# Performance work log

Hardware: AMD Instinct MI355X
Metric: run time of the kernel (lower is better)

## Reference

```python
import jax, jax.numpy as jnp
import numpy as np

B, S, D_IN, D_H = 2048, 256, 128, 256
C2 = 2.7193  # time-decay log offset from the original module


def setup_inputs() -> dict:
    key = jax.random.key(0)
    k0, k1, k2, k3 = jax.random.split(key, 4)
    inputs = jax.random.normal(k0, (B, S, D_IN), dtype=jnp.float32)
    # time must be increasing so intervals are positive (log(dt + 2.7193) valid)
    dt = jax.random.uniform(k1, (B, S), minval=0.1, maxval=5.0, dtype=jnp.float32)
    time = jnp.cumsum(dt, axis=1)
    Wi = jax.random.normal(k2, (D_IN, D_H), dtype=jnp.float32) / np.sqrt(D_IN).astype(np.float32)
    bi = jnp.zeros((D_H,), dtype=jnp.float32)
    Wh = jax.random.normal(k3, (D_H, D_H), dtype=jnp.float32) / np.sqrt(D_H).astype(np.float32)
    bh = jnp.zeros((D_H,), dtype=jnp.float32)
    return {"inputs": inputs, "time": time, "Wi": Wi, "bi": bi, "Wh": Wh, "bh": bh}


def reference(inputs, time, Wi, bi, Wh, bh):
    Bsz, Slen, _ = inputs.shape
    H = Wh.shape[0]
    # time points -> intervals, then decay weight 1/log(dt + c2)
    dt = time[:, 1:] - time[:, :-1]                     # [B, S-1]
    w = 1.0 / jnp.log(dt + C2)                          # [B, S-1]
    # precompute all input projections once (original recomputes per gate)
    x_proj = jnp.einsum('bsd,dh->bsh', inputs[:, :-1], Wi) + bi  # [B, S-1, H]

    def step(carry, xs):
        h, c, o = carry
        xz, wt = xs                                     # xz:[B,H], wt:[B]
        z = xz + h @ Wh + bh                            # shared gate pre-activation
        g = jax.nn.sigmoid(z)                           # f_t == i_t == o_t (same linears in source)
        C_bar = jnp.tanh(z)
        C_S = jnp.tanh(c @ Wh + bh)                     # short-term memory
        C_star = (c - C_S) + C_S * wt[:, None]          # long-term + discounted short-term
        c_new = g * C_star + g * C_bar
        h_new = g * jnp.tanh(C_bar)
        return (h_new, c_new, g), None

    zeros = jnp.zeros((Bsz, H), dtype=inputs.dtype)
    (h, c, o), _ = jax.lax.scan(
        step, (zeros, zeros, zeros),
        (jnp.swapaxes(x_proj, 0, 1), w.T),
    )
    res = o @ Wh + bh                                   # linear_hidden(o_t) of last step
    return jnp.stack((res, h, c))                       # [3, B, H]
```

## Files before the change

### kernel.cpp

```cpp
#include <hip/hip_runtime.h>

typedef __attribute__((ext_vector_type(8))) short short8;
typedef __attribute__((ext_vector_type(4))) float floatx4;
typedef __attribute__((ext_vector_type(2))) float floatx2;

#define LOG2E 1.44269504088896340736f

#define BAR() asm volatile("s_waitcnt lgkmcnt(0)\n\ts_barrier" ::: "memory")

__device__ __forceinline__ unsigned short f2bf(float f) {
  unsigned u = __float_as_uint(f);
  u += 0x7FFFu + ((u >> 16) & 1u);
  return (unsigned short)(u >> 16);
}

__device__ __forceinline__ unsigned cvtpk(float lo, float hi) {
  unsigned r;
  asm("v_cvt_pk_bf16_f32 %0, %1, %2" : "=v"(r) : "v"(lo), "v"(hi));
  return r;
}

__device__ __forceinline__ int sidx(int row, int k) {
  return row * 256 + (k ^ ((row & 7) << 3));
}

__global__ __launch_bounds__(1024, 4) void tlstm_kernel(
    const float* __restrict__ x, const float* __restrict__ tim,
    const float* __restrict__ Wi, const float* __restrict__ bi,
    const float* __restrict__ Wh, const float* __restrict__ bh,
    float* __restrict__ out)
{
  __shared__ __align__(16) unsigned short Sst[2 * 4096];
  __shared__ __align__(16) unsigned short Sx[2 * 2048];
  __shared__ float WMt[2048];

  const int tid = threadIdx.x;
  const int wv  = tid >> 6;
  const int l   = tid & 63;
  const int q   = l >> 4;
  const int r   = l & 15;
  const int b0  = blockIdx.x * 8;
  const int col = wv * 16 + r;

  short8 wh[8];
#pragma unroll
  for (int c = 0; c < 8; ++c)
#pragma unroll
    for (int j = 0; j < 8; ++j)
      wh[c][j] = (short)f2bf(Wh[(c * 32 + q * 8 + j) * 256 + col]);
  short8 wi[4];
#pragma unroll
  for (int c = 0; c < 4; ++c)
#pragma unroll
    for (int j = 0; j < 8; ++j)
      wi[c][j] = (short)f2bf(Wi[(c * 32 + q * 8 + j) * 256 + col]);
  const float bhc = bh[col], bic = bi[col];

  const int rbx = (r >> 2) & 1;
  const int Bs  = r * 256 + 8 * (q ^ (r & 3));
  const int raE = Bs + 32 * rbx;
  const int raO = Bs + 32 * (1 - rbx);
  const int Bx  = r * 128 + 8 * (q ^ (r & 3));
  const int xaE = Bx + 32 * rbx;
  const int xaO = Bx + 32 * (1 - rbx);
  const int wr0 = sidx(4 * q,     col), wr1 = sidx(4 * q + 1, col);
  const int wr2 = sidx(4 * q + 2, col), wr3 = sidx(4 * q + 3, col);
  const int xwi = wv * 128 + ((2 * l) ^ ((wv & 7) << 3));
  const float* xp = x + (long)(b0 + (wv >> 1)) * 32768 + (wv & 1) * 128 + l * 2;

  *(unsigned long long*)&Sst[tid * 4] = 0ULL;
  for (int i = tid; i < 2040; i += 1024) {
    int t = i >> 3, bl = i & 7;
    float t0 = tim[(b0 + bl) * 256 + t];
    float t1 = tim[(b0 + bl) * 256 + t + 1];
    WMt[i] = 1.f - 1.f / logf(t1 - t0 + 2.7193f);
  }
  {
    floatx2 v = *(const floatx2*)xp;
    *(unsigned*)&Sx[xwi] = cvtpk(v.x, v.y);
  }
  xp += 256;
  __syncthreads();

  float c0 = 0.f, c1 = 0.f, h0 = 0.f, h1 = 0.f, g0 = 0.f, g1 = 0.f;
  int xro = 0;
  int wmi = 2 * q;

  auto proc1 = [&](float z0, float cp0, float cin, float wmv,
                   float& cno, float& gno, float& hno, int ih, int ic, int woff) {
    float z  = fminf(fmaxf(z0,  -10.f), 10.f);
    float cp = fminf(fmaxf(cp0, -10.f), 10.f);
    float u  = __builtin_amdgcn_exp2f(-LOG2E * z);
    float u2 = u * u;
    float v  = __builtin_amdgcn_exp2f(-2.f * LOG2E * cp);
    float a1 = 1.f + u, a2 = 1.f + u2, a3 = 1.f + v;
    float p12 = a1 * a2;
    float D   = __builtin_amdgcn_rcpf(p12 * a3);
    float Da3 = D * a3;
    float g   = Da3 * a2;
    float ir2 = Da3 * a1;
    float ir3 = D * p12;
    float Cb  = fmaf(-u2, ir2, ir2);
    float Cs  = fmaf(-v, ir3, ir3);
    float Cstar = fmaf(-Cs, wmv, cin);
    float cn = g * (Cstar + Cb);
    float s = Cb * Cb;
    float P = fmaf(0.003592028f, s, -0.008863236f);
    P = fmaf(P, s, 0.021869488f);
    P = fmaf(P, s, -0.053968254f);
    P = fmaf(P, s, 0.133333333f);
    P = fmaf(P, s, -0.333333333f);
    P = fmaf(P, s, 1.0f);
    float hn = g * (Cb * P);
    Sst[woff + ih] = (unsigned short)((__float_as_uint(hn) + 0x8000u) >> 16);
    Sst[woff + ic] = (unsigned short)((__float_as_uint(cn) + 0x8000u) >> 16);
    cno = cn; gno = g; hno = hn;
  };

  auto dostep = [&](int roff, int woff, float xz0, float xz1, int wmoff) {
    short8 sf[8];
    sf[0] = *(const short8*)&Sst[roff + raE];
    sf[1] = *(const short8*)&Sst[roff + raO];
    sf[2] = *(const short8*)&Sst[roff + raE + 64];
    sf[3] = *(const short8*)&Sst[roff + raO + 64];
    sf[4] = *(const short8*)&Sst[roff + raE + 128];
    sf[5] = *(const short8*)&Sst[roff + raO + 128];
    sf[6] = *(const short8*)&Sst[roff + raE + 192];
    sf[7] = *(const short8*)&Sst[roff + raO + 192];
    floatx4 aP = {bhc, bhc, bhc, bhc};
    floatx4 aQ = {0.f, 0.f, 0.f, 0.f};
    aP = __builtin_amdgcn_mfma_f32_16x16x32_bf16(sf[0], wh[0], aP, 0, 0, 0);
    aQ = __builtin_amdgcn_mfma_f32_16x16x32_bf16(sf[1], wh[1], aQ, 0, 0, 0);
    aP = __builtin_amdgcn_mfma_f32_16x16x32_bf16(sf[2], wh[2], aP, 0, 0, 0);
    aQ = __builtin_amdgcn_mfma_f32_16x16x32_bf16(sf[3], wh[3], aQ, 0, 0, 0);
    aP = __builtin_amdgcn_mfma_f32_16x16x32_bf16(sf[4], wh[4], aP, 0, 0, 0);
    aQ = __builtin_amdgcn_mfma_f32_16x16x32_bf16(sf[5], wh[5], aQ, 0, 0, 0);
    aP = __builtin_amdgcn_mfma_f32_16x16x32_bf16(sf[6], wh[6], aP, 0, 0, 0);
    aQ = __builtin_amdgcn_mfma_f32_16x16x32_bf16(sf[7], wh[7], aQ, 0, 0, 0);
    floatx2 wmv = *(const floatx2*)&WMt[wmoff];
    float z0  = aP[0] + aQ[0] + xz0;
    float cp0 = aP[1] + aQ[1];
    float z1  = aP[2] + aQ[2] + xz1;
    float cp1 = aP[3] + aQ[3];
    proc1(z0, cp0, c0, wmv.x, c0, g0, h0, wr0, wr1, woff);
    proc1(z1, cp1, c1, wmv.y, c1, g1, h1, wr2, wr3, woff);
    BAR();
  };

  floatx4 xacc;
  auto loadx = [&]() {
    short8 xf[4];
    xf[0] = *(const short8*)&Sx[xro + xaE];
    xf[1] = *(const short8*)&Sx[xro + xaO];
    xf[2] = *(const short8*)&Sx[xro + xaE + 64];
    xf[3] = *(const short8*)&Sx[xro + xaO + 64];
    floatx4 a = {bic, bic, bic, bic};
    a = __builtin_amdgcn_mfma_f32_16x16x32_bf16(xf[0], wi[0], a, 0, 0, 0);
    a = __builtin_amdgcn_mfma_f32_16x16x32_bf16(xf[1], wi[1], a, 0, 0, 0);
    a = __builtin_amdgcn_mfma_f32_16x16x32_bf16(xf[2], wi[2], a, 0, 0, 0);
    a = __builtin_amdgcn_mfma_f32_16x16x32_bf16(xf[3], wi[3], a, 0, 0, 0);
    xacc = a;
  };

  for (int p = 0; p < 127; ++p) {
    floatx2 nv = *(const floatx2*)xp;
    xp += 256;
    loadx();
    dostep(0, 4096, xacc[0], xacc[2], wmi);
    *(unsigned*)&Sx[(xro ^ 2048) + xwi] = cvtpk(nv.x, nv.y);
    dostep(4096, 0, xacc[1], xacc[3], wmi + 8);
    xro ^= 2048;
    wmi += 16;
  }

  loadx();
  dostep(0, 4096, xacc[0], xacc[2], wmi);

  Sst[wr0] = f2bf(g0);  Sst[wr1] = 0;
  Sst[wr2] = f2bf(g1);  Sst[wr3] = 0;
  BAR();
  short8 gf[8];
  gf[0] = *(const short8*)&Sst[raE];
  gf[1] = *(const short8*)&Sst[raO];
  gf[2] = *(const short8*)&Sst[raE + 64];
  gf[3] = *(const short8*)&Sst[raO + 64];
  gf[4] = *(const short8*)&Sst[raE + 128];
  gf[5] = *(const short8*)&Sst[raO + 128];
  gf[6] = *(const short8*)&Sst[raE + 192];
  gf[7] = *(const short8*)&Sst[raO + 192];
  floatx4 res = {bhc, bhc, bhc, bhc};
#pragma unroll
  for (int c = 0; c < 8; ++c)
    res = __builtin_amdgcn_mfma_f32_16x16x32_bf16(gf[c], wh[c], res, 0, 0, 0);

  const long P  = 2048L * 256;
  const long o0 = (long)(b0 + 2 * q) * 256;
  const long o1 = (long)(b0 + 2 * q + 1) * 256;
  out[o0 + col]         = res[0];
  out[o1 + col]         = res[2];
  out[P + o0 + col]     = h0;
  out[P + o1 + col]     = h1;
  out[2 * P + o0 + col] = c0;
  out[2 * P + o1 + col] = c1;
}

extern "C" void kernel_launch(void* const* d_in, const int* in_sizes, int n_in,
                              void* d_out, int out_size, void* d_ws, size_t ws_size,
                              hipStream_t stream) {
  const float* xin = (const float*)d_in[0];
  const float* tim = (const float*)d_in[1];
  const float* Wi  = (const float*)d_in[2];
  const float* bi  = (const float*)d_in[3];
  const float* Wh  = (const float*)d_in[4];
  const float* bh  = (const float*)d_in[5];
  tlstm_kernel<<<dim3(256), dim3(1024), 0, stream>>>(xin, tim, Wi, bi, Wh, bh, (float*)d_out);
}
```

Before: 272.6 us.

## Halve batch rows per block and give each wave two column tiles

Each block now handles 4 batch rows with 512 threads (8 waves) instead of 8 rows with 1024 threads, and the grid doubles to 512 blocks. Each wave holds two 16-column tiles of Wh and Wi in registers and issues two independent MFMA chains per step, using only half the lanes' results. The aim is cheaper per-step barriers with fewer waves and more blocks spread across CUs. In exchange, half of the MFMA output is wasted and register pressure from the doubled weight fragments rises, which may limit occupancy.

```diff
diff --git a/kernel.cpp b/kernel.cpp
--- a/kernel.cpp
+++ b/kernel.cpp
@@ -20,57 +20,66 @@
   return r;
 }
 
-__device__ __forceinline__ int sidx(int row, int k) {
-  return row * 256 + (k ^ ((row & 7) << 3));
-}
-
-__global__ __launch_bounds__(1024, 4) void tlstm_kernel(
+__global__ __launch_bounds__(512, 4) void tlstm_kernel(
     const float* __restrict__ x, const float* __restrict__ tim,
     const float* __restrict__ Wi, const float* __restrict__ bi,
     const float* __restrict__ Wh, const float* __restrict__ bh,
     float* __restrict__ out)
 {
-  __shared__ __align__(16) unsigned short Sst[2 * 4096];
-  __shared__ __align__(16) unsigned short Sx[2 * 2048];
-  __shared__ float WMt[2048];
+  __shared__ __align__(16) unsigned short Sst[2 * 2048];
+  __shared__ __align__(16) unsigned short Sx[2 * 1024];
+  __shared__ __align__(16) float WMt[1024];
 
   const int tid = threadIdx.x;
   const int wv  = tid >> 6;
   const int l   = tid & 63;
   const int q   = l >> 4;
   const int r   = l & 15;
-  const int b0  = blockIdx.x * 8;
-  const int col = wv * 16 + r;
-
-  short8 wh[8];
-#pragma unroll
-  for (int c = 0; c < 8; ++c)
-#pragma unroll
-    for (int j = 0; j < 8; ++j)
-      wh[c][j] = (short)f2bf(Wh[(c * 32 + q * 8 + j) * 256 + col]);
-  short8 wi[4];
-#pragma unroll
-  for (int c = 0; c < 4; ++c)
-#pragma unroll
-    for (int j = 0; j < 8; ++j)
-      wi[c][j] = (short)f2bf(Wi[(c * 32 + q * 8 + j) * 256 + col]);
-  const float bhc = bh[col], bic = bi[col];
-
-  const int rbx = (r >> 2) & 1;
-  const int Bs  = r * 256 + 8 * (q ^ (r & 3));
-  const int raE = Bs + 32 * rbx;
-  const int raO = Bs + 32 * (1 - rbx);
-  const int Bx  = r * 128 + 8 * (q ^ (r & 3));
-  const int xaE = Bx + 32 * rbx;
-  const int xaO = Bx + 32 * (1 - rbx);
-  const int wr0 = sidx(4 * q,     col), wr1 = sidx(4 * q + 1, col);
-  const int wr2 = sidx(4 * q + 2, col), wr3 = sidx(4 * q + 3, col);
-  const int xwi = wv * 128 + ((2 * l) ^ ((wv & 7) << 3));
+  const int r8  = r & 7;
+  const int qt  = q >> 1;
+  const int q1  = q & 1;
+  const int b0  = blockIdx.x * 4;
+
+  const int col1 = wv * 32 + r;
+  const int col2 = col1 + 16;
+  const int wcol = wv * 32 + qt * 16 + r;
+
+  short8 wh[2][8];
+#pragma unroll
+  for (int tx = 0; tx < 2; ++tx)
+#pragma unroll
+    for (int c = 0; c < 8; ++c)
+#pragma unroll
+      for (int j = 0; j < 8; ++j)
+        wh[tx][c][j] = (short)f2bf(Wh[(c * 32 + q * 8 + j) * 256 + wv * 32 + tx * 16 + r]);
+  short8 wi[2][4];
+#pragma unroll
+  for (int tx = 0; tx < 2; ++tx)
+#pragma unroll
+    for (int c = 0; c < 4; ++c)
+#pragma unroll
+      for (int j = 0; j < 8; ++j)
+        wi[tx][c][j] = (short)f2bf(Wi[(c * 32 + q * 8 + j) * 256 + wv * 32 + tx * 16 + r]);
+  const float bh1 = bh[col1], bh2 = bh[col2];
+  const float bi1 = bi[col1], bi2 = bi[col2];
+
+  const int rbx = r8 >> 2;
+  const int Bs  = r8 * 256 + ((q * 8) ^ ((r8 & 3) << 3));
+  const int raE = Bs + 32 * rbx, raO = Bs + 32 * (1 - rbx);
+  const int Bx  = r8 * 128 + ((q * 8) ^ ((r8 & 3) << 3));
+  const int xaE = Bx + 32 * rbx, xaO = Bx + 32 * (1 - rbx);
+  const int R0 = 4 * q1;
+  const int wr0 = R0 * 256       + (wcol ^ (R0 << 3));
+  const int wr1 = (R0 + 1) * 256 + (wcol ^ ((R0 + 1) << 3));
+  const int wr2 = (R0 + 2) * 256 + (wcol ^ ((R0 + 2) << 3));
+  const int wr3 = (R0 + 3) * 256 + (wcol ^ ((R0 + 3) << 3));
+  const int xwi = wv * 128 + ((2 * l) ^ (wv << 3));
   const float* xp = x + (long)(b0 + (wv >> 1)) * 32768 + (wv & 1) * 128 + l * 2;
+  const int wm2 = 2 * q1;
 
   *(unsigned long long*)&Sst[tid * 4] = 0ULL;
-  for (int i = tid; i < 2040; i += 1024) {
-    int t = i >> 3, bl = i & 7;
+  for (int i = tid; i < 1020; i += 512) {
+    int t = i >> 2, bl = i & 3;
     float t0 = tim[(b0 + bl) * 256 + t];
     float t1 = tim[(b0 + bl) * 256 + t + 1];
     WMt[i] = 1.f - 1.f / logf(t1 - t0 + 2.7193f);
@@ -82,9 +91,9 @@
   xp += 256;
   __syncthreads();
 
-  float c0 = 0.f, c1 = 0.f, h0 = 0.f, h1 = 0.f, g0 = 0.f, g1 = 0.f;
+  float c0s = 0.f, c1s = 0.f, h0 = 0.f, h1 = 0.f, g0 = 0.f, g1 = 0.f;
   int xro = 0;
-  int wmi = 2 * q;
+  int wmi = 0;
 
   auto proc1 = [&](float z0, float cp0, float cin, float wmv,
                    float& cno, float& gno, float& hno, int ih, int ic, int woff) {
@@ -127,81 +136,88 @@
     sf[5] = *(const short8*)&Sst[roff + raO + 128];
     sf[6] = *(const short8*)&Sst[roff + raE + 192];
     sf[7] = *(const short8*)&Sst[roff + raO + 192];
-    floatx4 aP = {bhc, bhc, bhc, bhc};
-    floatx4 aQ = {0.f, 0.f, 0.f, 0.f};
-    aP = __builtin_amdgcn_mfma_f32_16x16x32_bf16(sf[0], wh[0], aP, 0, 0, 0);
-    aQ = __builtin_amdgcn_mfma_f32_16x16x32_bf16(sf[1], wh[1], aQ, 0, 0, 0);
-    aP = __builtin_amdgcn_mfma_f32_16x16x32_bf16(sf[2], wh[2], aP, 0, 0, 0);
-    aQ = __builtin_amdgcn_mfma_f32_16x16x32_bf16(sf[3], wh[3], aQ, 0, 0, 0);
-    aP = __builtin_amdgcn_mfma_f32_16x16x32_bf16(sf[4], wh[4], aP, 0, 0, 0);
-    aQ = __builtin_amdgcn_mfma_f32_16x16x32_bf16(sf[5], wh[5], aQ, 0, 0, 0);
-    aP = __builtin_amdgcn_mfma_f32_16x16x32_bf16(sf[6], wh[6], aP, 0, 0, 0);
-    aQ = __builtin_amdgcn_mfma_f32_16x16x32_bf16(sf[7], wh[7], aQ, 0, 0, 0);
-    floatx2 wmv = *(const floatx2*)&WMt[wmoff];
-    float z0  = aP[0] + aQ[0] + xz0;
-    float cp0 = aP[1] + aQ[1];
-    float z1  = aP[2] + aQ[2] + xz1;
-    float cp1 = aP[3] + aQ[3];
-    proc1(z0, cp0, c0, wmv.x, c0, g0, h0, wr0, wr1, woff);
-    proc1(z1, cp1, c1, wmv.y, c1, g1, h1, wr2, wr3, woff);
+    floatx4 a1 = {bh1, bh1, bh1, bh1};
+    floatx4 a2 = {bh2, bh2, bh2, bh2};
+#pragma unroll
+    for (int c = 0; c < 8; ++c) {
+      a1 = __builtin_amdgcn_mfma_f32_16x16x32_bf16(sf[c], wh[0][c], a1, 0, 0, 0);
+      a2 = __builtin_amdgcn_mfma_f32_16x16x32_bf16(sf[c], wh[1][c], a2, 0, 0, 0);
+    }
+    floatx2 wmv = *(const floatx2*)&WMt[wmoff + wm2];
+    float z0  = (qt ? a2[0] : a1[0]) + xz0;
+    float cp0 =  qt ? a2[1] : a1[1];
+    float z1  = (qt ? a2[2] : a1[2]) + xz1;
+    float cp1 =  qt ? a2[3] : a1[3];
+    proc1(z0, cp0, c0s, wmv.x, c0s, g0, h0, wr0, wr1, woff);
+    proc1(z1, cp1, c1s, wmv.y, c1s, g1, h1, wr2, wr3, woff);
     BAR();
   };
 
-  floatx4 xacc;
+  float xz[4];
   auto loadx = [&]() {
     short8 xf[4];
     xf[0] = *(const short8*)&Sx[xro + xaE];
     xf[1] = *(const short8*)&Sx[xro + xaO];
     xf[2] = *(const short8*)&Sx[xro + xaE + 64];
     xf[3] = *(const short8*)&Sx[xro + xaO + 64];
-    floatx4 a = {bic, bic, bic, bic};
-    a = __builtin_amdgcn_mfma_f32_16x16x32_bf16(xf[0], wi[0], a, 0, 0, 0);
-    a = __builtin_amdgcn_mfma_f32_16x16x32_bf16(xf[1], wi[1], a, 0, 0, 0);
-    a = __builtin_amdgcn_mfma_f32_16x16x32_bf16(xf[2], wi[2], a, 0, 0, 0);
-    a = __builtin_amdgcn_mfma_f32_16x16x32_bf16(xf[3], wi[3], a, 0, 0, 0);
-    xacc = a;
+    floatx4 x1 = {bi1, bi1, bi1, bi1};
+    floatx4 x2 = {bi2, bi2, bi2, bi2};
+#pragma unroll
+    for (int c = 0; c < 4; ++c) {
+      x1 = __builtin_amdgcn_mfma_f32_16x16x32_bf16(xf[c], wi[0][c], x1, 0, 0, 0);
+      x2 = __builtin_amdgcn_mfma_f32_16x16x32_bf16(xf[c], wi[1][c], x2, 0, 0, 0);
+    }
+    xz[0] = qt ? x2[0] : x1[0];
+    xz[1] = qt ? x2[1] : x1[1];
+    xz[2] = qt ? x2[2] : x1[2];
+    xz[3] = qt ? x2[3] : x1[3];
   };
 
   for (int p = 0; p < 127; ++p) {
     floatx2 nv = *(const floatx2*)xp;
     xp += 256;
     loadx();
-    dostep(0, 4096, xacc[0], xacc[2], wmi);
-    *(unsigned*)&Sx[(xro ^ 2048) + xwi] = cvtpk(nv.x, nv.y);
-    dostep(4096, 0, xacc[1], xacc[3], wmi + 8);
-    xro ^= 2048;
-    wmi += 16;
+    dostep(0, 2048, xz[0], xz[2], wmi);
+    *(unsigned*)&Sx[(xro ^ 1024) + xwi] = cvtpk(nv.x, nv.y);
+    dostep(2048, 0, xz[1], xz[3], wmi + 4);
+    xro ^= 1024;
+    wmi += 8;
   }
 
   loadx();
-  dostep(0, 4096, xacc[0], xacc[2], wmi);
-
-  Sst[wr0] = f2bf(g0);  Sst[wr1] = 0;
-  Sst[wr2] = f2bf(g1);  Sst[wr3] = 0;
+  dostep(0, 2048, xz[0], xz[2], wmi);
+
+  Sst[2048 + wr0] = f2bf(g0);  Sst[2048 + wr1] = 0;
+  Sst[2048 + wr2] = f2bf(g1);  Sst[2048 + wr3] = 0;
   BAR();
   short8 gf[8];
-  gf[0] = *(const short8*)&Sst[raE];
-  gf[1] = *(const short8*)&Sst[raO];
-  gf[2] = *(const short8*)&Sst[raE + 64];
-  gf[3] = *(const short8*)&Sst[raO + 64];
-  gf[4] = *(const short8*)&Sst[raE + 128];
-  gf[5] = *(const short8*)&Sst[raO + 128];
-  gf[6] = *(const short8*)&Sst[raE + 192];
-  gf[7] = *(const short8*)&Sst[raO + 192];
-  floatx4 res = {bhc, bhc, bhc, bhc};
-#pragma unroll
-  for (int c = 0; c < 8; ++c)
-    res = __builtin_amdgcn_mfma_f32_16x16x32_bf16(gf[c], wh[c], res, 0, 0, 0);
+  gf[0] = *(const short8*)&Sst[2048 + raE];
+  gf[1] = *(const short8*)&Sst[2048 + raO];
+  gf[2] = *(const short8*)&Sst[2048 + raE + 64];
+  gf[3] = *(const short8*)&Sst[2048 + raO + 64];
+  gf[4] = *(const short8*)&Sst[2048 + raE + 128];
+  gf[5] = *(const short8*)&Sst[2048 + raO + 128];
+  gf[6] = *(const short8*)&Sst[2048 + raE + 192];
+  gf[7] = *(const short8*)&Sst[2048 + raO + 192];
+  floatx4 r1 = {bh1, bh1, bh1, bh1};
+  floatx4 r2 = {bh2, bh2, bh2, bh2};
+#pragma unroll
+  for (int c = 0; c < 8; ++c) {
+    r1 = __builtin_amdgcn_mfma_f32_16x16x32_bf16(gf[c], wh[0][c], r1, 0, 0, 0);
+    r2 = __builtin_amdgcn_mfma_f32_16x16x32_bf16(gf[c], wh[1][c], r2, 0, 0, 0);
+  }
+  float res0 = qt ? r2[0] : r1[0];
+  float res2 = qt ? r2[2] : r1[2];
 
   const long P  = 2048L * 256;
-  const long o0 = (long)(b0 + 2 * q) * 256;
-  const long o1 = (long)(b0 + 2 * q + 1) * 256;
-  out[o0 + col]         = res[0];
-  out[o1 + col]         = res[2];
-  out[P + o0 + col]     = h0;
-  out[P + o1 + col]     = h1;
-  out[2 * P + o0 + col] = c0;
-  out[2 * P + o1 + col] = c1;
+  const long o0 = (long)(b0 + 2 * q1) * 256;
+  const long o1 = (long)(b0 + 2 * q1 + 1) * 256;
+  out[o0 + wcol]         = res0;
+  out[o1 + wcol]         = res2;
+  out[P + o0 + wcol]     = h0;
+  out[P + o1 + wcol]     = h1;
+  out[2 * P + o0 + wcol] = c0s;
+  out[2 * P + o1 + wcol] = c1s;
 }
 
 extern "C" void kernel_launch(void* const* d_in, const int* in_sizes, int n_in,
@@ -213,5 +229,5 @@
   const float* bi  = (const float*)d_in[3];
   const float* Wh  = (const float*)d_in[4];
   const float* bh  = (const float*)d_in[5];
-  tlstm_kernel<<<dim3(256), dim3(1024), 0, stream>>>(xin, tim, Wi, bi, Wh, bh, (float*)d_out);
-}
+  tlstm_kernel<<<dim3(512), dim3(512), 0, stream>>>(xin, tim, Wi, bi, Wh, bh, (float*)d_out);
+}
```

After: 678.9 us. 149% more time.
